# Performance work log

Measured on AMD Instinct MI355X. Metric: run time of the kernel, lower is better.

Reference implementation:

```python
import jax, jax.numpy as jnp
import numpy as np

B, S, D = 4, 1024, 1024
H = 16
DH = D // H           # 64
ROT = 64              # rotary_emb_dim (full head dim)
NEG_INF = -10000.0
ROPE_BASE = 10000.0


def _rope_tables(seqlen, rot_dim, dtype=jnp.float32):
    inv_freq = 1.0 / (ROPE_BASE ** (jnp.arange(0, rot_dim, 2, dtype=jnp.float32) / rot_dim))
    t = jnp.arange(seqlen, dtype=jnp.float32)
    freqs = jnp.einsum('s,f->sf', t, inv_freq)  # (S, rot_dim//2)
    return jnp.cos(freqs).astype(dtype), jnp.sin(freqs).astype(dtype)


def _apply_rotary(x, cos, sin):
    # x: (B, S, H, DH); GPT-NeoX (non-interleaved) rotary over first ROT dims
    half = ROT // 2
    x_rot, x_pass = x[..., :ROT], x[..., ROT:]
    x1, x2 = x_rot[..., :half], x_rot[..., half:]
    c = cos[None, :, None, :]
    s = sin[None, :, None, :]
    rot = jnp.concatenate([x1 * c - x2 * s, x2 * c + x1 * s], axis=-1)
    return jnp.concatenate([rot, x_pass], axis=-1) if x_pass.shape[-1] else rot


def setup_inputs() -> dict:
    key = jax.random.key(0)
    ks = jax.random.split(key, 5)
    sc_in = 1.0 / np.sqrt(D)
    return {
        'x': jax.random.normal(ks[0], (B, S, D), jnp.float32),
        'Wqkv': jax.random.normal(ks[1], (3 * D, D), jnp.float32) * sc_in,
        'bqkv': jax.random.normal(ks[2], (3 * D,), jnp.float32) * 0.01,
        'Wout': jax.random.normal(ks[3], (D, D), jnp.float32) * sc_in,
        'bout': jax.random.normal(ks[4], (D,), jnp.float32) * 0.01,
    }


def reference(x, Wqkv, bqkv, Wout, bout):
    # QKV projection: (B,S,D) -> (B,S,3,H,DH)
    qkv = (jnp.einsum('bsd,ed->bse', x, Wqkv) + bqkv).reshape(B, S, 3, H, DH)
    q, k, v = qkv[:, :, 0], qkv[:, :, 1], qkv[:, :, 2]
    cos, sin = _rope_tables(S, ROT, q.dtype)
    q = _apply_rotary(q, cos, sin)
    k = _apply_rotary(k, cos, sin)
    scale = 1.0 / np.sqrt(DH)
    scores = jnp.einsum('bthd,bshd->bhts', q, k * scale)  # (B,H,S,S)
    causal_mask = jnp.triu(jnp.full((S, S), NEG_INF, dtype=scores.dtype), 1)
    scores = scores + causal_mask
    attn = jax.nn.softmax(scores, axis=-1)
    out = jnp.einsum('bhts,bshd->bthd', attn, v).reshape(B, S, D)
    return jnp.einsum('bsd,ed->bse', out, Wout) + bout
```

## Files before the change

### kernel.cpp

```cpp
#include <hip/hip_runtime.h>

#define B_ 4
#define S_ 1024
#define D_ 1024
#define H_ 16
#define DH_ 64

typedef unsigned short u16;
typedef __attribute__((ext_vector_type(8))) short bf16x8;
typedef __attribute__((ext_vector_type(4))) float f32x4;

__device__ __forceinline__ float bf2f(u16 h){
  union { unsigned u; float f; } x; x.u = ((unsigned)h) << 16; return x.f;
}
__device__ __forceinline__ u16 f2bf(float f){
  union { float f; unsigned u; } x; x.f = f;
  unsigned u = x.u;
  return (u16)((u + 0x7fffu + ((u >> 16) & 1u)) >> 16);
}

__device__ __forceinline__ void gload16(const u16* g, u16* l){
  __builtin_amdgcn_global_load_lds(
      (const __attribute__((address_space(1))) unsigned int*)g,
      (__attribute__((address_space(3))) unsigned int*)l, 16, 0, 0);
}

__global__ __launch_bounds__(256) void cast3(
    const float* __restrict__ a, u16* __restrict__ oa, int na,
    const float* __restrict__ b, u16* __restrict__ ob, int nb,
    const float* __restrict__ c, u16* __restrict__ oc){
  int i = (blockIdx.x * 256 + threadIdx.x) * 4;
  const float* src; u16* dst;
  if (i < na){ src = a + i; dst = oa + i; }
  else if (i < na + nb){ src = b + (i - na); dst = ob + (i - na); }
  else { src = c + (i - na - nb); dst = oc + (i - na - nb); }
  float4 v = *(const float4*)src;
  union { u16 s[4]; uint2 u; } o;
  o.s[0] = f2bf(v.x); o.s[1] = f2bf(v.y); o.s[2] = f2bf(v.z); o.s[3] = f2bf(v.w);
  *(uint2*)dst = o.u;
}

__global__ __launch_bounds__(256) void rope_tab(float2* __restrict__ tab){
  int idx = blockIdx.x * 256 + threadIdx.x;
  int s = idx >> 5, i = idx & 31;
  float invf = powf(10000.0f, -(float)i * (1.0f / 32.0f));
  float sn, cs;
  sincosf((float)s * invf, &sn, &cs);
  tab[idx] = make_float2(cs, sn);
}

__global__ __launch_bounds__(512, 2) void gemm_qkv8(const u16* __restrict__ A,
    const u16* __restrict__ Bm, const float* __restrict__ bias,
    const float2* __restrict__ tab,
    u16* __restrict__ qb, u16* __restrict__ kb, u16* __restrict__ vtb){
  __shared__ u16 As_[2][2][128*64];
  __shared__ u16 Bs_[2][2][128*64];
  const int K = 1024;
  const int tid = threadIdx.x;
  const int lane = tid & 63, wid = tid >> 6;
  const int wr = wid >> 2, wc = wid & 3;
  const int lo = lane & 15, g = lane >> 4;

  const int bid = blockIdx.x;
  const int swz = (bid & 7) * 24 + (bid >> 3);
  const int bx = swz & 15, by = swz >> 4;
  const int m0 = bx * 256, n0 = by * 256;

  f32x4 acc[8][4];
  #pragma unroll
  for (int i = 0; i < 8; ++i)
    #pragma unroll
    for (int j = 0; j < 4; ++j) acc[i][j] = (f32x4){0.f, 0.f, 0.f, 0.f};

  auto stage = [&](int b, int kt){
    const u16* ga = A + (size_t)m0 * K + kt * 64;
    const u16* gb = Bm + (size_t)n0 * K + kt * 64;
    #pragma unroll
    for (int it = 0; it < 2; ++it){
      int c = tid + it * 512;
      int r = c >> 3;
      int colbs = ((c & 7) * 16) ^ ((r & 7) << 4);
      int src = r * K + (colbs >> 1);
      gload16(ga + src,           &As_[b][0][c * 8]);
      gload16(ga + 128*K + src,   &As_[b][1][c * 8]);
      gload16(gb + src,           &Bs_[b][0][c * 8]);
      gload16(gb + 128*K + src,   &Bs_[b][1][c * 8]);
    }
  };

  auto rdA = [&](int b, int qm, int fm, int ks) -> bf16x8 {
    int row = qm*64 + fm*16 + lo;
    int byte = row*128 + ((ks*64 + g*16) ^ ((lo & 7) << 4));
    return *(const bf16x8*)(&As_[b][wr][byte >> 1]);
  };
  auto rdB = [&](int b, int fn, int ks) -> bf16x8 {
    int row = (wc & 1)*64 + fn*16 + lo;
    int byte = row*128 + ((ks*64 + g*16) ^ ((lo & 7) << 4));
    return *(const bf16x8*)(&Bs_[b][wc >> 1][byte >> 1]);
  };

  auto ktile = [&](int b, int stage_t){
    bf16x8 a[8], bq[8];
    #pragma unroll
    for (int fm = 0; fm < 4; ++fm)
      #pragma unroll
      for (int ks = 0; ks < 2; ++ks) a[fm*2+ks] = rdA(b, 0, fm, ks);
    #pragma unroll
    for (int fn = 0; fn < 4; ++fn)
      #pragma unroll
      for (int ks = 0; ks < 2; ++ks) bq[fn*2+ks] = rdB(b, fn, ks);
    __builtin_amdgcn_s_setprio(1);
    #pragma unroll
    for (int fm = 0; fm < 4; ++fm)
      #pragma unroll
      for (int fn = 0; fn < 2; ++fn)
        #pragma unroll
        for (int ks = 0; ks < 2; ++ks)
          acc[fm][fn] = __builtin_amdgcn_mfma_f32_16x16x32_bf16(a[fm*2+ks], bq[fn*2+ks], acc[fm][fn], 0, 0, 0);
    __builtin_amdgcn_s_setprio(0);
    __builtin_amdgcn_s_setprio(1);
    #pragma unroll
    for (int fm = 0; fm < 4; ++fm)
      #pragma unroll
      for (int fn = 0; fn < 2; ++fn)
        #pragma unroll
        for (int ks = 0; ks < 2; ++ks)
          acc[fm][2+fn] = __builtin_amdgcn_mfma_f32_16x16x32_bf16(a[fm*2+ks], bq[(2+fn)*2+ks], acc[fm][2+fn], 0, 0, 0);
    __builtin_amdgcn_s_setprio(0);
    #pragma unroll
    for (int fm = 0; fm < 4; ++fm)
      #pragma unroll
      for (int ks = 0; ks < 2; ++ks) a[fm*2+ks] = rdA(b, 1, fm, ks);
    __builtin_amdgcn_s_setprio(1);
    #pragma unroll
    for (int fm = 0; fm < 4; ++fm)
      #pragma unroll
      for (int fn = 0; fn < 2; ++fn)
        #pragma unroll
        for (int ks = 0; ks < 2; ++ks)
          acc[4+fm][fn] = __builtin_amdgcn_mfma_f32_16x16x32_bf16(a[fm*2+ks], bq[fn*2+ks], acc[4+fm][fn], 0, 0, 0);
    __builtin_amdgcn_s_setprio(0);
    asm volatile("s_waitcnt lgkmcnt(0)" ::: "memory");
    __builtin_amdgcn_sched_barrier(0);
    __builtin_amdgcn_s_barrier();
    __builtin_amdgcn_sched_barrier(0);
    if (stage_t >= 0) stage(b, stage_t);
    __builtin_amdgcn_s_setprio(1);
    #pragma unroll
    for (int fm = 0; fm < 4; ++fm)
      #pragma unroll
      for (int fn = 0; fn < 2; ++fn)
        #pragma unroll
        for (int ks = 0; ks < 2; ++ks)
          acc[4+fm][2+fn] = __builtin_amdgcn_mfma_f32_16x16x32_bf16(a[fm*2+ks], bq[(2+fn)*2+ks], acc[4+fm][2+fn], 0, 0, 0);
    __builtin_amdgcn_s_setprio(0);
  };

  stage(0, 0);
  stage(1, 1);
  for (int t = 0; t < 14; ++t){
    asm volatile("s_waitcnt vmcnt(8)" ::: "memory");
    __builtin_amdgcn_s_barrier();
    __builtin_amdgcn_sched_barrier(0);
    ktile(t & 1, t + 2);
  }
  asm volatile("s_waitcnt vmcnt(8)" ::: "memory");
  __builtin_amdgcn_s_barrier();
  __builtin_amdgcn_sched_barrier(0);
  ktile(0, -1);
  asm volatile("s_waitcnt vmcnt(0)" ::: "memory");
  __builtin_amdgcn_s_barrier();
  __builtin_amdgcn_sched_barrier(0);
  ktile(1, -1);

  const int ty = by >> 2;
  const int h  = (by & 3) * 4 + wc;
  float bv[4];
  #pragma unroll
  for (int fn = 0; fn < 4; ++fn) bv[fn] = bias[n0 + wc*64 + fn*16 + lo];

  if (ty < 2){
    u16* dst = (ty == 0) ? qb : kb;
    #pragma unroll
    for (int fm = 0; fm < 8; ++fm){
      #pragma unroll
      for (int j = 0; j < 4; ++j){
        int row = m0 + wr*128 + fm*16 + g*4 + j;
        int bb = row >> 10, s = row & 1023;
        size_t obase = (((size_t)(bb * H_ + h)) * S_ + s) * DH_;
        #pragma unroll
        for (int fn = 0; fn < 2; ++fn){
          int i = fn*16 + lo;
          float2 t2 = tab[s*32 + i];
          float v1 = acc[fm][fn][j] + bv[fn];
          float v2 = acc[fm][fn+2][j] + bv[fn+2];
          dst[obase + i]      = f2bf(v1 * t2.x - v2 * t2.y);
          dst[obase + i + 32] = f2bf(v2 * t2.x + v1 * t2.y);
        }
      }
    }
  } else {
    __syncthreads();
    u16* wbase = (wid < 4) ? ((u16*)As_ + wid * 8192)
                           : ((u16*)Bs_ + (wid - 4) * 8192);
    #pragma unroll
    for (int fm = 0; fm < 8; ++fm)
      #pragma unroll
      for (int fn = 0; fn < 4; ++fn){
        int d = fn*16 + lo;
        #pragma unroll
        for (int j = 0; j < 4; ++j){
          int sl = fm*16 + g*4 + j;
          int sx = sl ^ ((d & 7) << 4);
          wbase[d*128 + sx] = f2bf(acc[fm][fn][j] + bv[fn]);
        }
      }
    const int rowblk = m0 + wr*128;
    const int bb = rowblk >> 10;
    const int sbase = rowblk & 1023;
    #pragma unroll
    for (int pass = 0; pass < 16; ++pass){
      int d = pass*4 + g;
      int sc = lo * 8;
      int sx = sc ^ ((d & 7) << 4);
      bf16x8 v = *(const bf16x8*)(&wbase[d*128 + sx]);
      *(bf16x8*)(vtb + (((size_t)(bb * H_ + h)) * DH_ + d) * S_ + sbase + sc) = v;
    }
  }
}

template<int OUT_BF16>
__global__ __launch_bounds__(256) void gemm_bt(const u16* __restrict__ A,
    const u16* __restrict__ Bm, const float* __restrict__ bias,
    void* __restrict__ Cout, int M, int N, int K){
  __shared__ u16 As[2][128*32];
  __shared__ u16 Bs[2][128*32];
  const int tid = threadIdx.x;
  const int lane = tid & 63;
  const int w = tid >> 6;
  const int wr = w >> 1, wc = w & 1;
  const int lo = lane & 15, g = lane >> 4;
  const int m0 = blockIdx.x * 128, n0 = blockIdx.y * 128;

  f32x4 acc[4][4];
  #pragma unroll
  for (int i = 0; i < 4; ++i)
    #pragma unroll
    for (int j = 0; j < 4; ++j) acc[i][j] = (f32x4){0.f, 0.f, 0.f, 0.f};

  const int nt = K >> 5;

  auto stage = [&](int buf, int kt){
    const u16* ga = A + (size_t)m0 * K + kt * 32;
    const u16* gb = Bm + (size_t)n0 * K + kt * 32;
    #pragma unroll
    for (int it = 0; it < 2; ++it){
      int chunk = tid + it * 256;
      int row = chunk >> 2;
      int c0 = (chunk & 3) * 8;
      gload16(ga + (size_t)row * K + c0, &As[buf][chunk * 8]);
      gload16(gb + (size_t)row * K + c0, &Bs[buf][chunk * 8]);
    }
  };

  stage(0, 0);
  __syncthreads();
  int buf = 0;
  for (int kt = 0; kt < nt; ++kt){
    if (kt + 1 < nt) stage(buf ^ 1, kt + 1);
    bf16x8 af[4], bfr[4];
    #pragma unroll
    for (int mi = 0; mi < 4; ++mi)
      af[mi] = *(const bf16x8*)(&As[buf][(wr*64 + mi*16 + lo)*32 + g*8]);
    #pragma unroll
    for (int ni = 0; ni < 4; ++ni)
      bfr[ni] = *(const bf16x8*)(&Bs[buf][(wc*64 + ni*16 + lo)*32 + g*8]);
    #pragma unroll
    for (int mi = 0; mi < 4; ++mi)
      #pragma unroll
      for (int ni = 0; ni < 4; ++ni)
        acc[mi][ni] = __builtin_amdgcn_mfma_f32_16x16x32_bf16(af[mi], bfr[ni], acc[mi][ni], 0, 0, 0);
    __syncthreads();
    buf ^= 1;
  }

  #pragma unroll
  for (int mi = 0; mi < 4; ++mi){
    int row = m0 + wr*64 + mi*16 + g*4;
    #pragma unroll
    for (int ni = 0; ni < 4; ++ni){
      int col = n0 + wc*64 + ni*16 + lo;
      float bvs = bias[col];
      #pragma unroll
      for (int j = 0; j < 4; ++j){
        float v = acc[mi][ni][j] + bvs;
        if (OUT_BF16) ((u16*)Cout)[(size_t)(row + j) * N + col] = f2bf(v);
        else          ((float*)Cout)[(size_t)(row + j) * N + col] = v;
      }
    }
  }
}

__global__ __launch_bounds__(512) void attn_fwd(const u16* __restrict__ qb,
    const u16* __restrict__ kb, const u16* __restrict__ vtb,
    u16* __restrict__ ctx){
  const int bh = blockIdx.x;
  const int qt = 7 - blockIdx.y;
  const int b = bh >> 4, h = bh & 15;
  const int tid = threadIdx.x;
  const int lane = tid & 63, w = tid >> 6;
  const int lo = lane & 15, g = lane >> 4;

  __shared__ u16 Kl[2][64*64];
  __shared__ u16 Vl[2][64*64];
  __shared__ u16 Plds[8][16][72];

  bf16x8 qf[2];
  {
    const u16* qa = qb + ((size_t)bh * S_ + qt*128 + w*16 + lo) * DH_ + g*8;
    qf[0] = *(const bf16x8*)(qa);  qf[1] = *(const bf16x8*)(qa + 32);
  }

  float m_run[4], l_run[4];
  f32x4 O[4];
  #pragma unroll
  for (int j = 0; j < 4; ++j){ m_run[j] = -1e30f; l_run[j] = 0.f; }
  #pragma unroll
  for (int c = 0; c < 4; ++c) O[c] = (f32x4){0.f,0.f,0.f,0.f};

  auto stage = [&](int buf, int kt){
    const u16* ksrc = kb  + ((size_t)bh * S_ + kt*64) * DH_;
    const u16* vsrc = vtb + (size_t)bh * DH_ * S_ + kt*64;
    int c = tid;
    int row = c >> 3;
    int colbs = ((c & 7) * 16) ^ ((row & 7) << 4);
    gload16(ksrc + (size_t)row * DH_ + (colbs >> 1), &Kl[buf][c * 8]);
    gload16(vsrc + (size_t)row * S_  + (colbs >> 1), &Vl[buf][c * 8]);
  };

  int buf = 0;

  auto computeTile = [&](int kt, bool diag){
    f32x4 sacc[4];
    #pragma unroll
    for (int c = 0; c < 4; ++c) sacc[c] = (f32x4){0.f,0.f,0.f,0.f};
    __builtin_amdgcn_s_setprio(1);
    #pragma unroll
    for (int cf = 0; cf < 4; ++cf){
      int r = cf*16 + lo;
      #pragma unroll
      for (int ks = 0; ks < 2; ++ks){
        int byteoff = r*128 + ((ks*64 + g*16) ^ ((lo & 7) << 4));
        bf16x8 kf = *(const bf16x8*)(&Kl[buf][byteoff >> 1]);
        sacc[cf] = __builtin_amdgcn_mfma_f32_16x16x32_bf16(qf[ks], kf, sacc[cf], 0, 0, 0);
      }
    }
    __builtin_amdgcn_s_setprio(0);
    #pragma unroll
    for (int cf = 0; cf < 4; ++cf){
      #pragma unroll
      for (int j = 0; j < 4; ++j){
        float sv = sacc[cf][j] * 0.125f;
        if (diag){
          int kj = kt*64 + cf*16 + lo;
          int qr = qt*128 + w*16 + g*4 + j;
          if (kj > qr) sv -= 10000.f;
        }
        sacc[cf][j] = sv;
      }
    }
    float mnew[4], alpha[4], rsum[4];
    #pragma unroll
    for (int j = 0; j < 4; ++j){
      float v = fmaxf(fmaxf(sacc[0][j], sacc[1][j]), fmaxf(sacc[2][j], sacc[3][j]));
      v = fmaxf(v, __shfl_xor(v, 1));
      v = fmaxf(v, __shfl_xor(v, 2));
      v = fmaxf(v, __shfl_xor(v, 4));
      v = fmaxf(v, __shfl_xor(v, 8));
      mnew[j] = fmaxf(m_run[j], v);
      alpha[j] = __expf(m_run[j] - mnew[j]);
      m_run[j] = mnew[j];
      rsum[j] = 0.f;
    }
    #pragma unroll
    for (int cf = 0; cf < 4; ++cf){
      #pragma unroll
      for (int j = 0; j < 4; ++j){
        float pv = __expf(sacc[cf][j] - mnew[j]);
        sacc[cf][j] = pv;
        rsum[j] += pv;
      }
    }
    #pragma unroll
    for (int j = 0; j < 4; ++j){
      float v = rsum[j];
      v += __shfl_xor(v, 1);
      v += __shfl_xor(v, 2);
      v += __shfl_xor(v, 4);
      v += __shfl_xor(v, 8);
      l_run[j] = l_run[j] * alpha[j] + v;
    }
    #pragma unroll
    for (int c = 0; c < 4; ++c)
      #pragma unroll
      for (int j = 0; j < 4; ++j) O[c][j] *= alpha[j];

    #pragma unroll
    for (int cf = 0; cf < 4; ++cf)
      #pragma unroll
      for (int j = 0; j < 4; ++j)
        Plds[w][g*4 + j][cf*16 + lo] = f2bf(sacc[cf][j]);

    __builtin_amdgcn_s_setprio(1);
    #pragma unroll
    for (int ks = 0; ks < 2; ++ks){
      bf16x8 pf = *(const bf16x8*)(&Plds[w][lo][ks*32 + g*8]);
      #pragma unroll
      for (int ocf = 0; ocf < 4; ++ocf){
        int r = ocf*16 + lo;
        int byteoff = r*128 + ((ks*64 + g*16) ^ ((lo & 7) << 4));
        bf16x8 vf = *(const bf16x8*)(&Vl[buf][byteoff >> 1]);
        O[ocf] = __builtin_amdgcn_mfma_f32_16x16x32_bf16(pf, vf, O[ocf], 0, 0, 0);
      }
    }
    __builtin_amdgcn_s_setprio(0);
  };

  const int nsteps = 2*qt + 2;
  stage(0, 0);
  for (int kt = 0; kt < nsteps; ++kt){
    __syncthreads();
    if (kt + 1 < nsteps) stage(buf ^ 1, kt + 1);
    computeTile(kt, kt >= 2*qt);
    buf ^= 1;
  }

  float inv[4];
  #pragma unroll
  for (int j = 0; j < 4; ++j) inv[j] = 1.0f / l_run[j];
  #pragma unroll
  for (int ocf = 0; ocf < 4; ++ocf){
    #pragma unroll
    for (int j = 0; j < 4; ++j){
      int d = ocf*16 + lo;
      int qi = qt*128 + w*16 + g*4 + j;
      ctx[((size_t)(b * S_ + qi)) * D_ + h * DH_ + d] = f2bf(O[ocf][j] * inv[j]);
    }
  }
}

extern "C" void kernel_launch(void* const* d_in, const int* in_sizes, int n_in,
                              void* d_out, int out_size, void* d_ws, size_t ws_size,
                              hipStream_t stream){
  (void)in_sizes; (void)n_in; (void)out_size; (void)ws_size;
  const float* x    = (const float*)d_in[0];
  const float* Wqkv = (const float*)d_in[1];
  const float* bqkv = (const float*)d_in[2];
  const float* Wout = (const float*)d_in[3];
  const float* bout = (const float*)d_in[4];
  float* out = (float*)d_out;

  char* p = (char*)d_ws;
  u16* x_bf    = (u16*)p; p += (size_t)4096*1024*2;
  u16* wqkv_bf = (u16*)p; p += (size_t)3072*1024*2;
  u16* wout_bf = (u16*)p; p += (size_t)1024*1024*2;
  u16* q_bf    = (u16*)p; p += (size_t)4096*1024*2;
  u16* k_bf    = (u16*)p; p += (size_t)4096*1024*2;
  u16* vt_bf   = (u16*)p; p += (size_t)4096*1024*2;
  u16* ctx_bf  = (u16*)p; p += (size_t)4096*1024*2;
  float2* tab  = (float2*)p; p += (size_t)1024*32*8;

  const int na = 4096*1024, nb = 3072*1024;
  cast3<<<8192, 256, 0, stream>>>(x, x_bf, na, Wqkv, wqkv_bf, nb, Wout, wout_bf);
  rope_tab<<<128, 256, 0, stream>>>(tab);

  gemm_qkv8<<<192, 512, 0, stream>>>(x_bf, wqkv_bf, bqkv, tab, q_bf, k_bf, vt_bf);

  attn_fwd<<<dim3(64, 8), 512, 0, stream>>>(q_bf, k_bf, vt_bf, ctx_bf);

  gemm_bt<0><<<dim3(32, 8), 256, 0, stream>>>(ctx_bf, wout_bf, bout, out, 4096, 1024, 1024);
}
```

Baseline: 113.0 us.

## Split QKV GEMM staging, shrink attention q-tiles, add lazy softmax rescale

Result: faster. 109.3 us (-3.3%).

```diff
diff --git a/kernel.cpp b/kernel.cpp
--- a/kernel.cpp
+++ b/kernel.cpp
@@ -72,20 +72,36 @@
     #pragma unroll
     for (int j = 0; j < 4; ++j) acc[i][j] = (f32x4){0.f, 0.f, 0.f, 0.f};
 
-  auto stage = [&](int b, int kt){
+  auto stage_p0 = [&](int b, int kt){
     const u16* ga = A + (size_t)m0 * K + kt * 64;
     const u16* gb = Bm + (size_t)n0 * K + kt * 64;
-    #pragma unroll
-    for (int it = 0; it < 2; ++it){
-      int c = tid + it * 512;
+    {
+      int c = tid;
       int r = c >> 3;
       int colbs = ((c & 7) * 16) ^ ((r & 7) << 4);
       int src = r * K + (colbs >> 1);
-      gload16(ga + src,           &As_[b][0][c * 8]);
-      gload16(ga + 128*K + src,   &As_[b][1][c * 8]);
-      gload16(gb + src,           &Bs_[b][0][c * 8]);
-      gload16(gb + 128*K + src,   &Bs_[b][1][c * 8]);
-    }
+      gload16(ga + src,         &As_[b][0][c * 8]);
+      gload16(ga + 128*K + src, &As_[b][1][c * 8]);
+      gload16(gb + src,         &Bs_[b][0][c * 8]);
+      gload16(gb + 128*K + src, &Bs_[b][1][c * 8]);
+    }
+    {
+      int c = tid + 512;
+      int r = c >> 3;
+      int colbs = ((c & 7) * 16) ^ ((r & 7) << 4);
+      int src = r * K + (colbs >> 1);
+      gload16(gb + src,         &Bs_[b][0][c * 8]);
+      gload16(gb + 128*K + src, &Bs_[b][1][c * 8]);
+    }
+  };
+  auto stage_p1 = [&](int b, int kt){
+    const u16* ga = A + (size_t)m0 * K + kt * 64;
+    int c = tid + 512;
+    int r = c >> 3;
+    int colbs = ((c & 7) * 16) ^ ((r & 7) << 4);
+    int src = r * K + (colbs >> 1);
+    gload16(ga + src,         &As_[b][0][c * 8]);
+    gload16(ga + 128*K + src, &As_[b][1][c * 8]);
   };
 
   auto rdA = [&](int b, int qm, int fm, int ks) -> bf16x8 {
@@ -118,6 +134,11 @@
         for (int ks = 0; ks < 2; ++ks)
           acc[fm][fn] = __builtin_amdgcn_mfma_f32_16x16x32_bf16(a[fm*2+ks], bq[fn*2+ks], acc[fm][fn], 0, 0, 0);
     __builtin_amdgcn_s_setprio(0);
+    asm volatile("s_waitcnt lgkmcnt(0)" ::: "memory");
+    __builtin_amdgcn_sched_barrier(0);
+    __builtin_amdgcn_s_barrier();
+    __builtin_amdgcn_sched_barrier(0);
+    if (stage_t >= 0) stage_p0(b, stage_t);
     __builtin_amdgcn_s_setprio(1);
     #pragma unroll
     for (int fm = 0; fm < 4; ++fm)
@@ -144,7 +165,7 @@
     __builtin_amdgcn_sched_barrier(0);
     __builtin_amdgcn_s_barrier();
     __builtin_amdgcn_sched_barrier(0);
-    if (stage_t >= 0) stage(b, stage_t);
+    if (stage_t >= 0) stage_p1(b, stage_t);
     __builtin_amdgcn_s_setprio(1);
     #pragma unroll
     for (int fm = 0; fm < 4; ++fm)
@@ -156,8 +177,8 @@
     __builtin_amdgcn_s_setprio(0);
   };
 
-  stage(0, 0);
-  stage(1, 1);
+  stage_p0(0, 0); stage_p1(0, 0);
+  stage_p0(1, 1); stage_p1(1, 1);
   for (int t = 0; t < 14; ++t){
     asm volatile("s_waitcnt vmcnt(8)" ::: "memory");
     __builtin_amdgcn_s_barrier();
@@ -301,11 +322,11 @@
   }
 }
 
-__global__ __launch_bounds__(512) void attn_fwd(const u16* __restrict__ qb,
+__global__ __launch_bounds__(256) void attn_fwd(const u16* __restrict__ qb,
     const u16* __restrict__ kb, const u16* __restrict__ vtb,
     u16* __restrict__ ctx){
   const int bh = blockIdx.x;
-  const int qt = 7 - blockIdx.y;
+  const int qt = 15 - blockIdx.y;
   const int b = bh >> 4, h = bh & 15;
   const int tid = threadIdx.x;
   const int lane = tid & 63, w = tid >> 6;
@@ -313,34 +334,39 @@
 
   __shared__ u16 Kl[2][64*64];
   __shared__ u16 Vl[2][64*64];
-  __shared__ u16 Plds[8][16][72];
-
-  bf16x8 qf[2];
-  {
-    const u16* qa = qb + ((size_t)bh * S_ + qt*128 + w*16 + lo) * DH_ + g*8;
-    qf[0] = *(const bf16x8*)(qa);  qf[1] = *(const bf16x8*)(qa + 32);
-  }
-
-  float m_run[4], l_run[4];
-  f32x4 O[4];
-  #pragma unroll
-  for (int j = 0; j < 4; ++j){ m_run[j] = -1e30f; l_run[j] = 0.f; }
-  #pragma unroll
-  for (int c = 0; c < 4; ++c) O[c] = (f32x4){0.f,0.f,0.f,0.f};
+  __shared__ u16 Plds[4][16][72];
 
   auto stage = [&](int buf, int kt){
     const u16* ksrc = kb  + ((size_t)bh * S_ + kt*64) * DH_;
     const u16* vsrc = vtb + (size_t)bh * DH_ * S_ + kt*64;
-    int c = tid;
-    int row = c >> 3;
-    int colbs = ((c & 7) * 16) ^ ((row & 7) << 4);
-    gload16(ksrc + (size_t)row * DH_ + (colbs >> 1), &Kl[buf][c * 8]);
-    gload16(vsrc + (size_t)row * S_  + (colbs >> 1), &Vl[buf][c * 8]);
-  };
+    #pragma unroll
+    for (int it = 0; it < 2; ++it){
+      int c = tid + it * 256;
+      int row = c >> 3;
+      int colbs = ((c & 7) * 16) ^ ((row & 7) << 4);
+      gload16(ksrc + (size_t)row * DH_ + (colbs >> 1), &Kl[buf][c * 8]);
+      gload16(vsrc + (size_t)row * S_  + (colbs >> 1), &Vl[buf][c * 8]);
+    }
+  };
+
+  stage(0, 0);
+
+  bf16x8 qf[2];
+  {
+    const u16* qa = qb + ((size_t)bh * S_ + qt*64 + w*16 + lo) * DH_ + g*8;
+    qf[0] = *(const bf16x8*)(qa);  qf[1] = *(const bf16x8*)(qa + 32);
+  }
+
+  float m_run[4], l_run[4];
+  f32x4 O[4];
+  #pragma unroll
+  for (int j = 0; j < 4; ++j){ m_run[j] = -1e30f; l_run[j] = 0.f; }
+  #pragma unroll
+  for (int c = 0; c < 4; ++c) O[c] = (f32x4){0.f,0.f,0.f,0.f};
 
   int buf = 0;
 
-  auto computeTile = [&](int kt, bool diag){
+  auto computeTile = [&](bool diag){
     f32x4 sacc[4];
     #pragma unroll
     for (int c = 0; c < 4; ++c) sacc[c] = (f32x4){0.f,0.f,0.f,0.f};
@@ -362,14 +388,14 @@
       for (int j = 0; j < 4; ++j){
         float sv = sacc[cf][j] * 0.125f;
         if (diag){
-          int kj = kt*64 + cf*16 + lo;
-          int qr = qt*128 + w*16 + g*4 + j;
+          int kj = cf*16 + lo;
+          int qr = w*16 + g*4 + j;
           if (kj > qr) sv -= 10000.f;
         }
         sacc[cf][j] = sv;
       }
     }
-    float mnew[4], alpha[4], rsum[4];
+    float rowmax[4];
     #pragma unroll
     for (int j = 0; j < 4; ++j){
       float v = fmaxf(fmaxf(sacc[0][j], sacc[1][j]), fmaxf(sacc[2][j], sacc[3][j]));
@@ -377,39 +403,71 @@
       v = fmaxf(v, __shfl_xor(v, 2));
       v = fmaxf(v, __shfl_xor(v, 4));
       v = fmaxf(v, __shfl_xor(v, 8));
-      mnew[j] = fmaxf(m_run[j], v);
-      alpha[j] = __expf(m_run[j] - mnew[j]);
-      m_run[j] = mnew[j];
-      rsum[j] = 0.f;
-    }
+      rowmax[j] = v;
+    }
+    float need = fmaxf(fmaxf(rowmax[0]-m_run[0], rowmax[1]-m_run[1]),
+                       fmaxf(rowmax[2]-m_run[2], rowmax[3]-m_run[3]));
+    float rsum[4] = {0.f,0.f,0.f,0.f};
+    if (__all(need <= 8.0f)){
+      #pragma unroll
+      for (int cf = 0; cf < 4; ++cf)
+        #pragma unroll
+        for (int j = 0; j < 4; ++j){
+          float pv = __expf(sacc[cf][j] - m_run[j]);
+          sacc[cf][j] = pv;
+          rsum[j] += pv;
+        }
+      #pragma unroll
+      for (int j = 0; j < 4; ++j){
+        float v = rsum[j];
+        v += __shfl_xor(v, 1);
+        v += __shfl_xor(v, 2);
+        v += __shfl_xor(v, 4);
+        v += __shfl_xor(v, 8);
+        l_run[j] += v;
+      }
+    } else {
+      float alpha[4];
+      #pragma unroll
+      for (int j = 0; j < 4; ++j){
+        float mnew = fmaxf(m_run[j], rowmax[j]);
+        alpha[j] = __expf(m_run[j] - mnew);
+        m_run[j] = mnew;
+      }
+      #pragma unroll
+      for (int cf = 0; cf < 4; ++cf)
+        #pragma unroll
+        for (int j = 0; j < 4; ++j){
+          float pv = __expf(sacc[cf][j] - m_run[j]);
+          sacc[cf][j] = pv;
+          rsum[j] += pv;
+        }
+      #pragma unroll
+      for (int j = 0; j < 4; ++j){
+        float v = rsum[j];
+        v += __shfl_xor(v, 1);
+        v += __shfl_xor(v, 2);
+        v += __shfl_xor(v, 4);
+        v += __shfl_xor(v, 8);
+        l_run[j] = l_run[j] * alpha[j] + v;
+      }
+      #pragma unroll
+      for (int c = 0; c < 4; ++c)
+        #pragma unroll
+        for (int j = 0; j < 4; ++j) O[c][j] *= alpha[j];
+    }
+
     #pragma unroll
     for (int cf = 0; cf < 4; ++cf){
       #pragma unroll
-      for (int j = 0; j < 4; ++j){
-        float pv = __expf(sacc[cf][j] - mnew[j]);
-        sacc[cf][j] = pv;
-        rsum[j] += pv;
-      }
-    }
-    #pragma unroll
-    for (int j = 0; j < 4; ++j){
-      float v = rsum[j];
-      v += __shfl_xor(v, 1);
-      v += __shfl_xor(v, 2);
-      v += __shfl_xor(v, 4);
-      v += __shfl_xor(v, 8);
-      l_run[j] = l_run[j] * alpha[j] + v;
-    }
-    #pragma unroll
-    for (int c = 0; c < 4; ++c)
-      #pragma unroll
-      for (int j = 0; j < 4; ++j) O[c][j] *= alpha[j];
-
-    #pragma unroll
-    for (int cf = 0; cf < 4; ++cf)
-      #pragma unroll
-      for (int j = 0; j < 4; ++j)
-        Plds[w][g*4 + j][cf*16 + lo] = f2bf(sacc[cf][j]);
+      for (int jp = 0; jp < 2; ++jp){
+        unsigned pk;
+        asm("v_cvt_pk_bf16_f32 %0, %1, %2"
+            : "=v"(pk) : "v"(sacc[cf][jp*2]), "v"(sacc[cf][jp*2+1]));
+        Plds[w][g*4 + jp*2][cf*16 + lo]     = (u16)(pk & 0xffffu);
+        Plds[w][g*4 + jp*2 + 1][cf*16 + lo] = (u16)(pk >> 16);
+      }
+    }
 
     __builtin_amdgcn_s_setprio(1);
     #pragma unroll
@@ -426,12 +484,10 @@
     __builtin_amdgcn_s_setprio(0);
   };
 
-  const int nsteps = 2*qt + 2;
-  stage(0, 0);
-  for (int kt = 0; kt < nsteps; ++kt){
+  for (int kt = 0; kt <= qt; ++kt){
     __syncthreads();
-    if (kt + 1 < nsteps) stage(buf ^ 1, kt + 1);
-    computeTile(kt, kt >= 2*qt);
+    if (kt < qt) stage(buf ^ 1, kt + 1);
+    computeTile(kt == qt);
     buf ^= 1;
   }
 
@@ -443,7 +499,7 @@
     #pragma unroll
     for (int j = 0; j < 4; ++j){
       int d = ocf*16 + lo;
-      int qi = qt*128 + w*16 + g*4 + j;
+      int qi = qt*64 + w*16 + g*4 + j;
       ctx[((size_t)(b * S_ + qi)) * D_ + h * DH_ + d] = f2bf(O[ocf][j] * inv[j]);
     }
   }
@@ -476,7 +532,7 @@
 
   gemm_qkv8<<<192, 512, 0, stream>>>(x_bf, wqkv_bf, bqkv, tab, q_bf, k_bf, vt_bf);
 
-  attn_fwd<<<dim3(64, 8), 512, 0, stream>>>(q_bf, k_bf, vt_bf, ctx_bf);
+  attn_fwd<<<dim3(64, 16), 256, 0, stream>>>(q_bf, k_bf, vt_bf, ctx_bf);
 
   gemm_bt<0><<<dim3(32, 8), 256, 0, stream>>>(ctx_bf, wout_bf, bout, out, 4096, 1024, 1024);
 }
```
